# Optimization experiments

Measured on AMD Instinct MI355X. Metric: run time of the kernel, lower is better.

Reference implementation:

```python
import jax, jax.numpy as jnp
import numpy as np

N_OBJ = 100000
E = 2000000
F_OBJ = 8
NUM_REL = 51


def _linear_params(key, fan_in, fan_out):
    kw, kb = jax.random.split(key)
    bound = 1.0 / np.sqrt(fan_in)
    W = jax.random.uniform(kw, (fan_in, fan_out), jnp.float32, -bound, bound)
    b = jax.random.uniform(kb, (fan_out,), jnp.float32, -bound, bound)
    return W, b


def setup_inputs() -> dict:
    key = jax.random.key(0)
    ks = jax.random.split(key, 10)
    inp = {
        "object_features": jax.random.normal(ks[0], (N_OBJ, F_OBJ), jnp.float32),
        "relations": jax.random.randint(ks[1], (E,), 0, NUM_REL, jnp.int64) if jax.config.jax_enable_x64 else jax.random.randint(ks[1], (E,), 0, NUM_REL, jnp.int32),
        "relation_pairs": jax.random.randint(ks[2], (E, 2), 0, N_OBJ, jnp.int32),
    }
    # object_fc: 16->128->64->32->16 ; relation_fc: 16->8->4->NUM_REL
    dims_obj = [16, 128, 64, 32, 16]
    dims_rel = [16, 8, 4, NUM_REL]
    for i in range(4):
        W, b = _linear_params(ks[3 + i], dims_obj[i], dims_obj[i + 1])
        inp[f"oW{i}"] = W
        inp[f"ob{i}"] = b
    for i in range(3):
        W, b = _linear_params(ks[7 + i], dims_rel[i], dims_rel[i + 1])
        inp[f"rW{i}"] = W
        inp[f"rb{i}"] = b
    return inp


def reference(object_features, relations, relation_pairs,
              oW0, ob0, oW1, ob1, oW2, ob2, oW3, ob3,
              rW0, rb0, rW1, rb1, rW2, rb2):
    # Batched gather over all edges: [E, 16]
    h = jnp.concatenate([object_features[relation_pairs[:, 0]],
                         object_features[relation_pairs[:, 1]]], axis=-1)
    # object_fc: Linear+ReLU x3, final Linear
    h = jax.nn.relu(h @ oW0 + ob0)   # [E,128]
    h = jax.nn.relu(h @ oW1 + ob1)   # [E,64]
    h = jax.nn.relu(h @ oW2 + ob2)   # [E,32]
    h = h @ oW3 + ob3                # [E,16]
    # relation_fc
    h = jax.nn.relu(h @ rW0 + rb0)   # [E,8]
    h = jax.nn.relu(h @ rW1 + rb1)   # [E,4]
    out = h @ rW2 + rb2              # [E,NUM_REL]
    return out, relations
```

## Files before the change

### kernel.cpp

```cpp
#include <hip/hip_runtime.h>


typedef __attribute__((ext_vector_type(8))) short bf16x8;
typedef __attribute__((ext_vector_type(4))) float f32x4;

#define UNROLL _Pragma("unroll")

__device__ __forceinline__ unsigned fbits(float x) {
    union { float f; unsigned u; } v; v.f = x; return v.u;
}
__device__ __forceinline__ unsigned pk2t(float a, float b) {
    return (fbits(a) >> 16) | (fbits(b) & 0xffff0000u);
}
__device__ __forceinline__ unsigned short bf16rne(float x) {
    unsigned u = fbits(x);
    unsigned r = u + 0x7fffu + ((u >> 16) & 1u);
    return (unsigned short)(r >> 16);
}

__device__ __forceinline__ f32x4 mfma1(bf16x8 a, bf16x8 b, f32x4 acc) {
    return __builtin_amdgcn_mfma_f32_16x16x32_bf16(a, b, acc, 0, 0, 0);
}

__device__ __forceinline__ f32x4 bias4(const float* __restrict__ b, int nt, int g) {
    const float4 v = *(const float4*)(b + nt * 16 + g * 4);
    f32x4 r; r[0] = v.x; r[1] = v.y; r[2] = v.z; r[3] = v.w; return r;
}

__device__ __forceinline__ void chunk_store(unsigned short* __restrict__ tile,
                                            int lr, int klb, f32x4 a) {
    uint2 v; v.x = pk2t(a[0], a[1]); v.y = pk2t(a[2], a[3]);
    const int lanep = lr + 16 * (klb >> 3);
    *(uint2*)(tile + lanep * 8 + (klb & 7)) = v;
}

__device__ __forceinline__ void seed_bias_rows(unsigned short* __restrict__ tile,
                                               int g, int lr) {
    if (g == 0) {
        uint4 c2; c2.x = 0x3f80u; c2.y = 0; c2.z = 0; c2.w = 0;
        *(uint4*)(tile + (lr + 32) * 8) = c2;
    } else if (g == 1) {
        uint4 zz; zz.x = zz.y = zz.z = zz.w = 0;
        *(uint4*)(tile + (lr + 48) * 8) = zz;
    }
}

__global__ __launch_bounds__(256) void sg_prep(
    const float* __restrict__ oW0, const float* __restrict__ ob0,
    const float* __restrict__ oW1, const float* __restrict__ oW2,
    const float* __restrict__ oW3,
    const float* __restrict__ rW0, const float* __restrict__ rb0,
    const float* __restrict__ rW1, const float* __restrict__ rb1,
    const float* __restrict__ rW2, const float* __restrict__ rb2,
    unsigned short* __restrict__ wsp)
{
    const int idx = blockIdx.x * 256 + threadIdx.x;
    if (idx >= 17920) return;
    if (idx >= 16896) {
        const int t2 = idx - 16896;
        const int tile = t2 >> 9;
        const int l = (t2 >> 3) & 63, j = t2 & 7;
        const int k = (l >> 4) * 8 + j;
        const int n = l & 15;
        float v = 0.0f;
        if (tile == 0) {
            if (n < 8) { if (k < 16) v = rW0[k * 8 + n]; else if (k == 16) v = rb0[n]; }
        } else {
            if (n < 4) { if (k < 8) v = rW1[k * 4 + n]; else if (k == 16) v = rb1[n]; }
        }
        wsp[idx] = bf16rne(v);
        return;
    }
    if (idx >= 14848) {
        const int t2 = idx - 14848;
        const int nt = t2 >> 9;
        const int l = (t2 >> 3) & 63, j = t2 & 7;
        const int k = (l >> 4) * 8 + j;
        const int n = nt * 16 + (l & 15);
        float v = 0.0f;
        if (n < 51) {
            if (k < 4)       v = rW2[k * 51 + n];
            else if (k == 4) v = rb2[n];
        }
        wsp[idx] = bf16rne(v);
        return;
    }
    int t = idx, K, N, kt, nt;
    const float* W;
    bool isW0 = false;
    if (t < 4096)        { W = oW0; K = 16;  N = 128; kt = 0; nt = t >> 9; isW0 = true; }
    else if (t < 12288)  { t -= 4096;  W = oW1; K = 128; N = 64; int f = t >> 9; kt = f >> 2; nt = f & 3; }
    else if (t < 14336)  { t -= 12288; W = oW2; K = 64;  N = 32; int f = t >> 9; kt = f >> 1; nt = f & 1; }
    else                 { t -= 14336; W = oW3; K = 32;  N = 16; kt = 0; nt = 0; }
    const int lid = (t >> 3) & 63, j = t & 7;
    const int k = kt * 32 + (lid >> 4) * 8 + j;
    const int n = nt * 16 + (lid & 15);
    float w = 0.0f;
    if (k < K)                w = W[(size_t)k * N + n];
    else if (isW0 && k == 16) w = ob0[n];
    wsp[idx] = bf16rne(w);
}

__global__ __launch_bounds__(256, 4) void sg_mfma(
    const float* __restrict__ obj, const int* __restrict__ rel,
    const int* __restrict__ pairs,
    const unsigned short* __restrict__ wsp,
    const float* __restrict__ ob1, const float* __restrict__ ob2,
    const float* __restrict__ ob3,
    float* __restrict__ out, float* __restrict__ out_rel, int E)
{
    __shared__ unsigned char smem[4 * 4096];
    const int tid = threadIdx.x;
    const int lid = tid & 63;
    const int wid = tid >> 6;
    const int g = lid >> 4, lr = lid & 15;
    unsigned short* sF = (unsigned short*)(smem + wid * 4096);

    const long long eBase = (long long)blockIdx.x * 256;
    const long long ee = eBase + tid;
    const int e = (ee < E) ? (int)ee : (E - 1);

    {
        const int2 pr = *(const int2*)(pairs + 2 * e);
        const float4* pa = (const float4*)(obj + (size_t)pr.x * 8);
        const float4* pb = (const float4*)(obj + (size_t)pr.y * 8);
        const float4 v0 = pa[0], v1 = pa[1], v2 = pb[0], v3 = pb[1];
        uint4 c0, c1, c2, zz;
        c0.x = pk2t(v0.x, v0.y); c0.y = pk2t(v0.z, v0.w);
        c0.z = pk2t(v1.x, v1.y); c0.w = pk2t(v1.z, v1.w);
        c1.x = pk2t(v2.x, v2.y); c1.y = pk2t(v2.z, v2.w);
        c1.z = pk2t(v3.x, v3.y); c1.w = pk2t(v3.z, v3.w);
        c2.x = 0x3f80u; c2.y = 0; c2.z = 0; c2.w = 0;
        zz.x = zz.y = zz.z = zz.w = 0;
        unsigned short* dh = sF + g * 512 + lr * 8;
        *(uint4*)(dh)       = c0;
        *(uint4*)(dh + 128) = c1;
        *(uint4*)(dh + 256) = c2;
        *(uint4*)(dh + 384) = zz;
    }

    bf16x8 a0[4];
    UNROLL for (int m = 0; m < 4; ++m)
        a0[m] = *(const bf16x8*)(sF + m * 512 + lid * 8);

    f32x4 acc2[4][4];
    UNROLL for (int m = 0; m < 4; ++m)
        UNROLL for (int n2 = 0; n2 < 4; ++n2) acc2[m][n2] = bias4(ob1, n2, g);

    for (int kt2 = 0; kt2 < 4; ++kt2) {
        UNROLL for (int m = 0; m < 4; ++m) {
            UNROLL for (int ntl = 0; ntl < 2; ++ntl) {
                const int nt = kt2 * 2 + ntl;
                f32x4 a = {0.0f, 0.0f, 0.0f, 0.0f};
                a = mfma1(*(const bf16x8*)(wsp + (size_t)nt * 512 + lid * 8), a0[m], a);
                UNROLL for (int jr = 0; jr < 4; ++jr) a[jr] = fmaxf(a[jr], 0.0f);
                chunk_store(sF + m * 512, lr, ntl * 16 + g * 4, a);
            }
        }
        UNROLL for (int m = 0; m < 4; ++m) {
            bf16x8 ah = *(const bf16x8*)(sF + m * 512 + lid * 8);
            UNROLL for (int n2 = 0; n2 < 4; ++n2) {
                const bf16x8 w = *(const bf16x8*)(wsp + 4096 + (size_t)(kt2 * 4 + n2) * 512 + lid * 8);
                acc2[m][n2] = mfma1(w, ah, acc2[m][n2]);
            }
        }
    }

    UNROLL for (int m = 0; m < 4; ++m)
        UNROLL for (int n2 = 0; n2 < 4; ++n2)
            UNROLL for (int jr = 0; jr < 4; ++jr)
                acc2[m][n2][jr] = fmaxf(acc2[m][n2][jr], 0.0f);

    f32x4 acc3[4][2];
    UNROLL for (int m = 0; m < 4; ++m)
        UNROLL for (int n3 = 0; n3 < 2; ++n3) acc3[m][n3] = bias4(ob2, n3, g);

    UNROLL for (int kt3 = 0; kt3 < 2; ++kt3) {
        UNROLL for (int m = 0; m < 4; ++m)
            UNROLL for (int ntl = 0; ntl < 2; ++ntl)
                chunk_store(sF + m * 512, lr, ntl * 16 + g * 4, acc2[m][2 * kt3 + ntl]);
        UNROLL for (int m = 0; m < 4; ++m) {
            bf16x8 ah = *(const bf16x8*)(sF + m * 512 + lid * 8);
            UNROLL for (int n3 = 0; n3 < 2; ++n3) {
                const bf16x8 w = *(const bf16x8*)(wsp + 12288 + (size_t)(kt3 * 2 + n3) * 512 + lid * 8);
                acc3[m][n3] = mfma1(w, ah, acc3[m][n3]);
            }
        }
    }

    UNROLL for (int m = 0; m < 4; ++m) {
        UNROLL for (int n3 = 0; n3 < 2; ++n3) {
            UNROLL for (int jr = 0; jr < 4; ++jr)
                acc3[m][n3][jr] = fmaxf(acc3[m][n3][jr], 0.0f);
            chunk_store(sF + m * 512, lr, n3 * 16 + g * 4, acc3[m][n3]);
        }
    }
    f32x4 acc4[4];
    UNROLL for (int m = 0; m < 4; ++m) {
        bf16x8 ah = *(const bf16x8*)(sF + m * 512 + lid * 8);
        acc4[m] = mfma1(*(const bf16x8*)(wsp + 14336 + lid * 8), ah, bias4(ob3, 0, g));
    }

    const bf16x8 w5 = *(const bf16x8*)(wsp + 16896 + lid * 8);
    const bf16x8 w6 = *(const bf16x8*)(wsp + 17408 + lid * 8);

    UNROLL for (int m = 0; m < 4; ++m) {
        chunk_store(sF + m * 512, lr, g * 4, acc4[m]);
        seed_bias_rows(sF + m * 512, g, lr);
    }
    f32x4 acc5[4];
    UNROLL for (int m = 0; m < 4; ++m) {
        bf16x8 b5 = *(const bf16x8*)(sF + m * 512 + lid * 8);
        f32x4 z = {0.0f, 0.0f, 0.0f, 0.0f};
        acc5[m] = mfma1(w5, b5, z);
        UNROLL for (int r = 0; r < 4; ++r) acc5[m][r] = fmaxf(acc5[m][r], 0.0f);
    }

    UNROLL for (int m = 0; m < 4; ++m) {
        chunk_store(sF + m * 512, lr, g * 4, acc5[m]);
        seed_bias_rows(sF + m * 512, g, lr);
    }
    f32x4 acc6[4];
    UNROLL for (int m = 0; m < 4; ++m) {
        bf16x8 b6 = *(const bf16x8*)(sF + m * 512 + lid * 8);
        f32x4 z = {0.0f, 0.0f, 0.0f, 0.0f};
        acc6[m] = mfma1(w6, b6, z);
        UNROLL for (int r = 0; r < 4; ++r) acc6[m][r] = fmaxf(acc6[m][r], 0.0f);
    }

    UNROLL for (int mt = 0; mt < 4; ++mt) {
        union { bf16x8 v; uint4 u; } afu;
        afu.u.x = pk2t(acc6[mt][0], acc6[mt][1]);
        afu.u.y = pk2t(acc6[mt][2], acc6[mt][3]);
        afu.u.z = (lid < 16) ? 0x00003f80u : 0u;
        afu.u.w = 0u;
        const long long erow = eBase + (long long)wid * 64 + mt * 16 + g * 4;
        UNROLL for (int nt = 0; nt < 4; ++nt) {
            f32x4 c = {0.0f, 0.0f, 0.0f, 0.0f};
            c = mfma1(afu.v, *(const bf16x8*)(wsp + 14848 + (size_t)nt * 512 + lid * 8), c);
            const int colv = nt * 16 + lr;
            UNROLL for (int r = 0; r < 4; ++r) {
                const long long ge = erow + r;
                if (colv < 51 && ge < E) out[ge * 51 + colv] = c[r];
            }
        }
    }

    if (ee < E) out_rel[ee] = (float)rel[e];
}

extern "C" void kernel_launch(void* const* d_in, const int* in_sizes, int n_in,
                              void* d_out, int out_size, void* d_ws, size_t ws_size,
                              hipStream_t stream) {
    const float* obj   = (const float*)d_in[0];
    const int*   rel   = (const int*)  d_in[1];
    const int*   pairs = (const int*)  d_in[2];
    const float* oW0 = (const float*)d_in[3];
    const float* ob0 = (const float*)d_in[4];
    const float* oW1 = (const float*)d_in[5];
    const float* ob1 = (const float*)d_in[6];
    const float* oW2 = (const float*)d_in[7];
    const float* ob2 = (const float*)d_in[8];
    const float* oW3 = (const float*)d_in[9];
    const float* ob3 = (const float*)d_in[10];
    const float* rW0 = (const float*)d_in[11];
    const float* rb0 = (const float*)d_in[12];
    const float* rW1 = (const float*)d_in[13];
    const float* rb1 = (const float*)d_in[14];
    const float* rW2 = (const float*)d_in[15];
    const float* rb2 = (const float*)d_in[16];

    const int E = in_sizes[1];
    float* out     = (float*)d_out;
    float* out_rel = out + (size_t)E * 51;
    unsigned short* wsp = (unsigned short*)d_ws;

    hipLaunchKernelGGL(sg_prep, dim3(70), dim3(256), 0, stream,
                       oW0, ob0, oW1, oW2, oW3,
                       rW0, rb0, rW1, rb1, rW2, rb2, wsp);

    const int blocks = (E + 255) / 256;
    hipLaunchKernelGGL(sg_mfma, dim3(blocks), dim3(256), 0, stream,
                       obj, rel, pairs, wsp,
                       ob1, ob2, ob3,
                       out, out_rel, E);
}
```

Before: 206.0 us.

## Halve edges per wave to cut registers and raise occupancy

Each wave now processes 32 edges (two 16-row M tiles) instead of 64, so accumulator arrays shrink by half and LDS per wave drops to 2KB. Launch bounds go from 4 to 8 waves-per-SIMD hint, and the block count doubles. Half the lanes do the gather while the rest seed the bias/zero rows. The w5/w6 weight loads are no longer held in registers across layers. The aim is to hide gather and memory latency through higher occupancy, at the cost of less weight-fragment reuse per MFMA and more global weight loads per edge.

```diff
diff --git a/kernel.cpp b/kernel.cpp
--- a/kernel.cpp
+++ b/kernel.cpp
@@ -101,7 +101,7 @@
     wsp[idx] = bf16rne(w);
 }
 
-__global__ __launch_bounds__(256, 4) void sg_mfma(
+__global__ __launch_bounds__(256, 8) void sg_mfma(
     const float* __restrict__ obj, const int* __restrict__ rel,
     const int* __restrict__ pairs,
     const unsigned short* __restrict__ wsp,
@@ -109,46 +109,49 @@
     const float* __restrict__ ob3,
     float* __restrict__ out, float* __restrict__ out_rel, int E)
 {
-    __shared__ unsigned char smem[4 * 4096];
+    __shared__ unsigned char smem[4 * 2048];
     const int tid = threadIdx.x;
     const int lid = tid & 63;
     const int wid = tid >> 6;
     const int g = lid >> 4, lr = lid & 15;
-    unsigned short* sF = (unsigned short*)(smem + wid * 4096);
-
-    const long long eBase = (long long)blockIdx.x * 256;
-    const long long ee = eBase + tid;
-    const int e = (ee < E) ? (int)ee : (E - 1);
-
-    {
+    unsigned short* sF = (unsigned short*)(smem + wid * 2048);
+
+    const int blockBase = blockIdx.x * 128;
+    const int wbase = blockBase + wid * 32;
+
+    if (g < 2) {
+        int e = wbase + g * 16 + lr;
+        if (e >= E) e = E - 1;
         const int2 pr = *(const int2*)(pairs + 2 * e);
         const float4* pa = (const float4*)(obj + (size_t)pr.x * 8);
         const float4* pb = (const float4*)(obj + (size_t)pr.y * 8);
         const float4 v0 = pa[0], v1 = pa[1], v2 = pb[0], v3 = pb[1];
-        uint4 c0, c1, c2, zz;
+        uint4 c0, c1;
         c0.x = pk2t(v0.x, v0.y); c0.y = pk2t(v0.z, v0.w);
         c0.z = pk2t(v1.x, v1.y); c0.w = pk2t(v1.z, v1.w);
         c1.x = pk2t(v2.x, v2.y); c1.y = pk2t(v2.z, v2.w);
         c1.z = pk2t(v3.x, v3.y); c1.w = pk2t(v3.z, v3.w);
-        c2.x = 0x3f80u; c2.y = 0; c2.z = 0; c2.w = 0;
-        zz.x = zz.y = zz.z = zz.w = 0;
         unsigned short* dh = sF + g * 512 + lr * 8;
         *(uint4*)(dh)       = c0;
         *(uint4*)(dh + 128) = c1;
-        *(uint4*)(dh + 256) = c2;
-        *(uint4*)(dh + 384) = zz;
-    }
-
-    bf16x8 a0[4];
-    UNROLL for (int m = 0; m < 4; ++m)
+    } else {
+        unsigned short* tile = sF + (g - 2) * 512;
+        uint4 c2; c2.x = 0x3f80u; c2.y = 0; c2.z = 0; c2.w = 0;
+        uint4 zz; zz.x = zz.y = zz.z = zz.w = 0;
+        *(uint4*)(tile + (lr + 32) * 8) = c2;
+        *(uint4*)(tile + (lr + 48) * 8) = zz;
+    }
+
+    bf16x8 a0[2];
+    UNROLL for (int m = 0; m < 2; ++m)
         a0[m] = *(const bf16x8*)(sF + m * 512 + lid * 8);
 
-    f32x4 acc2[4][4];
-    UNROLL for (int m = 0; m < 4; ++m)
+    f32x4 acc2[2][4];
+    UNROLL for (int m = 0; m < 2; ++m)
         UNROLL for (int n2 = 0; n2 < 4; ++n2) acc2[m][n2] = bias4(ob1, n2, g);
 
     for (int kt2 = 0; kt2 < 4; ++kt2) {
-        UNROLL for (int m = 0; m < 4; ++m) {
+        UNROLL for (int m = 0; m < 2; ++m) {
             UNROLL for (int ntl = 0; ntl < 2; ++ntl) {
                 const int nt = kt2 * 2 + ntl;
                 f32x4 a = {0.0f, 0.0f, 0.0f, 0.0f};
@@ -157,7 +160,7 @@
                 chunk_store(sF + m * 512, lr, ntl * 16 + g * 4, a);
             }
         }
-        UNROLL for (int m = 0; m < 4; ++m) {
+        UNROLL for (int m = 0; m < 2; ++m) {
             bf16x8 ah = *(const bf16x8*)(sF + m * 512 + lid * 8);
             UNROLL for (int n2 = 0; n2 < 4; ++n2) {
                 const bf16x8 w = *(const bf16x8*)(wsp + 4096 + (size_t)(kt2 * 4 + n2) * 512 + lid * 8);
@@ -166,20 +169,20 @@
         }
     }
 
-    UNROLL for (int m = 0; m < 4; ++m)
+    UNROLL for (int m = 0; m < 2; ++m)
         UNROLL for (int n2 = 0; n2 < 4; ++n2)
             UNROLL for (int jr = 0; jr < 4; ++jr)
                 acc2[m][n2][jr] = fmaxf(acc2[m][n2][jr], 0.0f);
 
-    f32x4 acc3[4][2];
-    UNROLL for (int m = 0; m < 4; ++m)
+    f32x4 acc3[2][2];
+    UNROLL for (int m = 0; m < 2; ++m)
         UNROLL for (int n3 = 0; n3 < 2; ++n3) acc3[m][n3] = bias4(ob2, n3, g);
 
     UNROLL for (int kt3 = 0; kt3 < 2; ++kt3) {
-        UNROLL for (int m = 0; m < 4; ++m)
+        UNROLL for (int m = 0; m < 2; ++m)
             UNROLL for (int ntl = 0; ntl < 2; ++ntl)
                 chunk_store(sF + m * 512, lr, ntl * 16 + g * 4, acc2[m][2 * kt3 + ntl]);
-        UNROLL for (int m = 0; m < 4; ++m) {
+        UNROLL for (int m = 0; m < 2; ++m) {
             bf16x8 ah = *(const bf16x8*)(sF + m * 512 + lid * 8);
             UNROLL for (int n3 = 0; n3 < 2; ++n3) {
                 const bf16x8 w = *(const bf16x8*)(wsp + 12288 + (size_t)(kt3 * 2 + n3) * 512 + lid * 8);
@@ -188,65 +191,63 @@
         }
     }
 
-    UNROLL for (int m = 0; m < 4; ++m) {
+    UNROLL for (int m = 0; m < 2; ++m) {
         UNROLL for (int n3 = 0; n3 < 2; ++n3) {
             UNROLL for (int jr = 0; jr < 4; ++jr)
                 acc3[m][n3][jr] = fmaxf(acc3[m][n3][jr], 0.0f);
             chunk_store(sF + m * 512, lr, n3 * 16 + g * 4, acc3[m][n3]);
         }
     }
-    f32x4 acc4[4];
-    UNROLL for (int m = 0; m < 4; ++m) {
+    f32x4 acc4[2];
+    UNROLL for (int m = 0; m < 2; ++m) {
         bf16x8 ah = *(const bf16x8*)(sF + m * 512 + lid * 8);
         acc4[m] = mfma1(*(const bf16x8*)(wsp + 14336 + lid * 8), ah, bias4(ob3, 0, g));
     }
 
-    const bf16x8 w5 = *(const bf16x8*)(wsp + 16896 + lid * 8);
-    const bf16x8 w6 = *(const bf16x8*)(wsp + 17408 + lid * 8);
-
-    UNROLL for (int m = 0; m < 4; ++m) {
+    UNROLL for (int m = 0; m < 2; ++m) {
         chunk_store(sF + m * 512, lr, g * 4, acc4[m]);
         seed_bias_rows(sF + m * 512, g, lr);
     }
-    f32x4 acc5[4];
-    UNROLL for (int m = 0; m < 4; ++m) {
+    f32x4 acc5[2];
+    UNROLL for (int m = 0; m < 2; ++m) {
         bf16x8 b5 = *(const bf16x8*)(sF + m * 512 + lid * 8);
         f32x4 z = {0.0f, 0.0f, 0.0f, 0.0f};
-        acc5[m] = mfma1(w5, b5, z);
+        acc5[m] = mfma1(*(const bf16x8*)(wsp + 16896 + lid * 8), b5, z);
         UNROLL for (int r = 0; r < 4; ++r) acc5[m][r] = fmaxf(acc5[m][r], 0.0f);
     }
 
-    UNROLL for (int m = 0; m < 4; ++m) {
+    UNROLL for (int m = 0; m < 2; ++m) {
         chunk_store(sF + m * 512, lr, g * 4, acc5[m]);
         seed_bias_rows(sF + m * 512, g, lr);
     }
-    f32x4 acc6[4];
-    UNROLL for (int m = 0; m < 4; ++m) {
+    f32x4 acc6[2];
+    UNROLL for (int m = 0; m < 2; ++m) {
         bf16x8 b6 = *(const bf16x8*)(sF + m * 512 + lid * 8);
         f32x4 z = {0.0f, 0.0f, 0.0f, 0.0f};
-        acc6[m] = mfma1(w6, b6, z);
+        acc6[m] = mfma1(*(const bf16x8*)(wsp + 17408 + lid * 8), b6, z);
         UNROLL for (int r = 0; r < 4; ++r) acc6[m][r] = fmaxf(acc6[m][r], 0.0f);
     }
 
-    UNROLL for (int mt = 0; mt < 4; ++mt) {
+    UNROLL for (int mt = 0; mt < 2; ++mt) {
         union { bf16x8 v; uint4 u; } afu;
         afu.u.x = pk2t(acc6[mt][0], acc6[mt][1]);
         afu.u.y = pk2t(acc6[mt][2], acc6[mt][3]);
         afu.u.z = (lid < 16) ? 0x00003f80u : 0u;
         afu.u.w = 0u;
-        const long long erow = eBase + (long long)wid * 64 + mt * 16 + g * 4;
+        const int erow = wbase + mt * 16 + g * 4;
         UNROLL for (int nt = 0; nt < 4; ++nt) {
             f32x4 c = {0.0f, 0.0f, 0.0f, 0.0f};
             c = mfma1(afu.v, *(const bf16x8*)(wsp + 14848 + (size_t)nt * 512 + lid * 8), c);
             const int colv = nt * 16 + lr;
             UNROLL for (int r = 0; r < 4; ++r) {
-                const long long ge = erow + r;
-                if (colv < 51 && ge < E) out[ge * 51 + colv] = c[r];
-            }
-        }
-    }
-
-    if (ee < E) out_rel[ee] = (float)rel[e];
+                const int ge = erow + r;
+                if (colv < 51 && ge < E) out[(size_t)ge * 51 + colv] = c[r];
+            }
+        }
+    }
+
+    const int re = blockBase + tid;
+    if (tid < 128 && re < E) out_rel[re] = (float)rel[re];
 }
 
 extern "C" void kernel_launch(void* const* d_in, const int* in_sizes, int n_in,
@@ -279,7 +280,7 @@
                        oW0, ob0, oW1, oW2, oW3,
                        rW0, rb0, rW1, rb1, rW2, rb2, wsp);
 
-    const int blocks = (E + 255) / 256;
+    const int blocks = (E + 127) / 128;
     hipLaunchKernelGGL(sg_mfma, dim3(blocks), dim3(256), 0, stream,
                        obj, rel, pairs, wsp,
                        ob1, ob2, ob3,
```

After: 397.3 us. 1.93x slower.
